# Performance work log

Hardware: AMD Instinct MI355X
Metric: run time of the kernel (lower is better)

Reference implementation:

```python
import jax, jax.numpy as jnp
import numpy as np

HEADS = 16
GROUPS = 4


def setup_inputs() -> dict:
    key = jax.random.key(0)
    k1, k2, k3, k4 = jax.random.split(key, 4)
    d_model = 2048
    d_kv = d_model * GROUPS // HEADS  # 512
    x = jax.random.normal(k1, (2, 2048, d_model), dtype=jnp.float32)
    Wq = jax.random.normal(k2, (d_model, d_model), dtype=jnp.float32) * (d_model ** -0.5)
    Wk = jax.random.normal(k3, (d_kv, d_model), dtype=jnp.float32) * (d_model ** -0.5)
    Wv = jax.random.normal(k4, (d_kv, d_model), dtype=jnp.float32) * (d_model ** -0.5)
    return {"x": x, "Wq": Wq, "Wk": Wk, "Wv": Wv}


def reference(x, Wq, Wk, Wv):
    b, t, c = x.shape
    hd = c // HEADS  # head dim
    h2g = HEADS // GROUPS  # query heads per kv group
    # projections (nn.Linear applies x @ W.T)
    q = (x @ Wq.T).reshape(b, t, HEADS, hd).transpose(0, 2, 1, 3)   # [b,H,t,hd]
    k = (x @ Wk.T).reshape(b, t, GROUPS, hd).transpose(0, 2, 1, 3)  # [b,G,t,hd]
    v = (x @ Wv.T).reshape(b, t, GROUPS, hd).transpose(0, 2, 1, 3)  # [b,G,t,hd]
    # GQA broadcast: group query heads by kv group
    qg = q.reshape(b, GROUPS, h2g, t, hd)                            # [b,G,h2g,t,hd]
    scores = jnp.einsum('bghqd,bgkd->bghqk', qg, k) * (hd ** -0.5)  # [b,G,h2g,t,t]
    causal = jnp.tril(jnp.ones((t, t), dtype=bool))
    scores = jnp.where(causal, scores, -jnp.inf)
    weights = jax.nn.softmax(scores, axis=-1)
    out = jnp.einsum('bghqk,bgkd->bghqd', weights, v)               # [b,G,h2g,t,hd]
    out = out.reshape(b, HEADS, t, hd).transpose(0, 2, 1, 3).reshape(b, t, c)
    return out
```

## Files before the change

kernel.cpp:

```cpp
#include <hip/hip_runtime.h>
#include <hip/hip_bf16.h>

typedef __bf16 bf16x8 __attribute__((ext_vector_type(8)));
typedef float f32x4 __attribute__((ext_vector_type(4)));

#define MFMA16(a,b,c) __builtin_amdgcn_mfma_f32_16x16x32_bf16(a,b,c,0,0,0)
#define GLL16(src, dst) __builtin_amdgcn_global_load_lds( \
    (const __attribute__((address_space(1))) unsigned int*)(src), \
    (__attribute__((address_space(3))) unsigned int*)(dst), 16, 0, 0)

__device__ inline unsigned int pack_bf16(float a, float b) {
    unsigned short ua = __builtin_bit_cast(unsigned short, (__bf16)a);
    unsigned short ub = __builtin_bit_cast(unsigned short, (__bf16)b);
    return ((unsigned int)ub << 16) | ua;
}
__device__ inline short bf_s(float v) {
    __bf16 b = (__bf16)v;
    return __builtin_bit_cast(short, b);
}

__global__ void cvt_all(const float* __restrict__ x,  const float* __restrict__ wq,
                        const float* __restrict__ wk, const float* __restrict__ wv,
                        __bf16* __restrict__ xb, __bf16* __restrict__ wb) {
    long i = (long)(blockIdx.x * blockDim.x + threadIdx.x) * 8;
    const float* src; __bf16* dst;
    if (i < 8388608)       { src = x  + i;              dst = xb + i; }
    else if (i < 12582912) { src = wq + (i - 8388608);  dst = wb + (i - 8388608); }
    else if (i < 13631488) { src = wk + (i - 12582912); dst = wb + (i - 12582912 + 4194304); }
    else                   { src = wv + (i - 13631488); dst = wb + (i - 13631488 + 5242880); }
    float4 a = *(const float4*)src;
    float4 b = *(const float4*)(src + 4);
    bf16x8 r;
    r[0] = (__bf16)a.x; r[1] = (__bf16)a.y; r[2] = (__bf16)a.z; r[3] = (__bf16)a.w;
    r[4] = (__bf16)b.x; r[5] = (__bf16)b.y; r[6] = (__bf16)b.z; r[7] = (__bf16)b.w;
    *(bf16x8*)dst = r;
}

__global__ __launch_bounds__(256) void gemm_qkv(const __bf16* __restrict__ A,
                                                const __bf16* __restrict__ B,
                                                __bf16* __restrict__ Qb,
                                                __bf16* __restrict__ Kf,
                                                __bf16* __restrict__ Vf,
                                                float qscale) {
    const int K = 2048;
    __shared__ __bf16 As[3 * 4096];
    __shared__ __bf16 Bs[3 * 4096];

    int tid = threadIdx.x;
    int wave = tid >> 6, lane = tid & 63;
    int quad = lane >> 4, l16 = lane & 15;

    int tm = blockIdx.x & 31, tn = blockIdx.x >> 5;

    const __bf16* Abase = A + (size_t)tm * 128 * K + (size_t)l16 * K + quad * 8;
    const __bf16* Bbase = B + (size_t)tn * 128 * K + (size_t)l16 * K + quad * 8;

    f32x4 acc[4][4] = {};

    auto stage = [&](int kt, int buf) {
#pragma unroll
        for (int rr = 0; rr < 2; ++rr) {
            int fb = rr * 4 + wave;
            GLL16(Abase + (size_t)fb * 16 * K + kt, As + buf * 4096 + fb * 512 + lane * 8);
            GLL16(Bbase + (size_t)fb * 16 * K + kt, Bs + buf * 4096 + fb * 512 + lane * 8);
        }
    };

    const int nk = K >> 5;
    stage(0, 0);
    stage(32, 1);
    asm volatile("s_waitcnt vmcnt(4)" ::: "memory");
    __builtin_amdgcn_s_barrier();

    int sl = 0, s2 = 2;
    for (int it = 0; it < nk; ++it) {
        if (it + 2 < nk) stage((it + 2) << 5, s2);
        const __bf16* Ab = As + sl * 4096;
        const __bf16* Bb = Bs + sl * 4096;
        bf16x8 af[4], bfr[4];
#pragma unroll
        for (int i = 0; i < 4; ++i)
            af[i] = *(const bf16x8*)(Ab + ((wave >> 1) * 4 + i) * 512 + lane * 8);
#pragma unroll
        for (int j = 0; j < 4; ++j)
            bfr[j] = *(const bf16x8*)(Bb + ((wave & 1) * 4 + j) * 512 + lane * 8);
#pragma unroll
        for (int i = 0; i < 4; ++i)
#pragma unroll
            for (int j = 0; j < 4; ++j)
                acc[i][j] = MFMA16(af[i], bfr[j], acc[i][j]);
        if (it + 1 < nk) {
            if (it + 2 < nk) asm volatile("s_waitcnt vmcnt(4)" ::: "memory");
            else             asm volatile("s_waitcnt vmcnt(0)" ::: "memory");
            __builtin_amdgcn_s_barrier();
        }
        sl = (sl == 2) ? 0 : sl + 1;
        s2 = (s2 == 2) ? 0 : s2 + 1;
    }

    int colbase = tn * 128 + (wave & 1) * 64;
#pragma unroll
    for (int i = 0; i < 4; ++i) {
        int row0 = tm * 128 + (wave >> 1) * 64 + i * 16 + quad * 4;
        int b = row0 >> 11, tok0 = row0 & 2047;
#pragma unroll
        for (int j = 0; j < 4; ++j) {
            int col = colbase + j * 16 + l16;
            if (tn < 16) {
#pragma unroll
                for (int r = 0; r < 4; ++r)
                    Qb[(size_t)(row0 + r) * 2048 + col] = (__bf16)(acc[i][j][r] * qscale);
            } else if (tn < 20) {
                int d_all = col - 2048;
                int g = d_all >> 7, dd = d_all & 127;
                int dt = dd >> 5, q4 = (dd >> 3) & 3, jj = dd & 7;
                int tb = tok0 >> 4, tl0 = tok0 & 15;
                __bf16* base = Kf + ((((size_t)(b * 4 + g) * 128 + tb) * 4 + dt) * 512)
                               + (q4 * 16 + tl0) * 8 + jj;
#pragma unroll
                for (int r = 0; r < 4; ++r)
                    base[r * 8] = (__bf16)acc[i][j][r];
            } else {
                int d_all = col - 2560;
                int g = d_all >> 7, dd = d_all & 127;
                int nto = dd >> 4, dl = dd & 15;
                int ch = tok0 >> 6, kk = (tok0 >> 5) & 1;
                int q4v = (tok0 >> 3) & 3, jv0 = tok0 & 7;
                size_t off = ((((size_t)(b * 4 + g) * 32 + ch) * 16) + nto * 2 + kk) * 512
                             + (q4v * 16 + dl) * 8 + jv0;
                short4 pk;
                pk.x = bf_s(acc[i][j][0]); pk.y = bf_s(acc[i][j][1]);
                pk.z = bf_s(acc[i][j][2]); pk.w = bf_s(acc[i][j][3]);
                *(short4*)(Vf + off) = pk;
            }
        }
    }
}

__global__ __launch_bounds__(256) void attn_mfma(const __bf16* __restrict__ Q,
                                                 const __bf16* __restrict__ Kf,
                                                 const __bf16* __restrict__ Vf,
                                                 float* __restrict__ O) {
    const int T = 2048, CM = 2048, HD = 128;
    __shared__ __bf16 Ks[2 * 8192];
    __shared__ __bf16 Vs[2 * 8192];
    __shared__ __bf16 Pl[8192];

    int tid = threadIdx.x;
    int wave = tid >> 6, lane = tid & 63;
    int quad = lane >> 4, l16 = lane & 15;

    int bg = blockIdx.x & 7;
    int slot = blockIdx.x >> 3;
    int qb = (slot < 32) ? (63 - slot) : (slot - 32);
    int b = bg >> 2, g = bg & 3;
    int h = g * 4 + wave;
    int q0 = qb * 32;

    bf16x8 qf[2][4];
    const __bf16* qbase = Q + (size_t)b * T * CM + (size_t)h * HD;
#pragma unroll
    for (int nt = 0; nt < 2; ++nt)
#pragma unroll
        for (int dt = 0; dt < 4; ++dt)
            qf[nt][dt] = *(const bf16x8*)(qbase + (size_t)(q0 + nt * 16 + l16) * CM
                                          + dt * 32 + quad * 8);

    const __bf16* kcb = Kf + (size_t)(b * 4 + g) * 262144;
    const __bf16* vcb = Vf + (size_t)(b * 4 + g) * 262144;

    float m_r[2] = {-1e30f, -1e30f}, l_r[2] = {0.f, 0.f};
    f32x4 o_acc[2][8] = {};
    __bf16* Pw = Pl + wave * 2048;

    auto stage_kv = [&](int ch, int buf) {
        const __bf16* kg = kcb + ch * 8192 + wave * 2048 + lane * 8;
        const __bf16* vg = vcb + ch * 8192 + wave * 2048 + lane * 8;
        __bf16* kl = Ks + buf * 8192 + wave * 2048 + lane * 8;
        __bf16* vl = Vs + buf * 8192 + wave * 2048 + lane * 8;
#pragma unroll
        for (int i = 0; i < 4; ++i) GLL16(kg + i * 512, kl + i * 512);
#pragma unroll
        for (int i = 0; i < 4; ++i) GLL16(vg + i * 512, vl + i * 512);
    };

    int nch = (qb >> 1) + 1;
    stage_kv(0, 0);
    for (int ch = 0; ch < nch; ++ch) {
        __builtin_amdgcn_s_barrier();
        if (ch + 1 < nch) {
            stage_kv(ch + 1, (ch + 1) & 1);
            asm volatile("s_waitcnt vmcnt(8)" ::: "memory");
        } else {
            asm volatile("s_waitcnt vmcnt(0)" ::: "memory");
        }
        __builtin_amdgcn_s_barrier();

        const __bf16* Kb = Ks + (ch & 1) * 8192;
        const __bf16* Vb = Vs + (ch & 1) * 8192;

        f32x4 st[2][4] = {};
#pragma unroll
        for (int t = 0; t < 4; ++t)
#pragma unroll
            for (int dt = 0; dt < 4; ++dt) {
                bf16x8 kfv = *(const bf16x8*)(Kb + (t * 4 + dt) * 512 + lane * 8);
                st[0][t] = MFMA16(kfv, qf[0][dt], st[0][t]);
                st[1][t] = MFMA16(kfv, qf[1][dt], st[1][t]);
            }

        bool diag = (ch == nch - 1);
        float alpha[2];
#pragma unroll
        for (int nt = 0; nt < 2; ++nt) {
            if (diag) {
                int qg = q0 + nt * 16 + l16;
#pragma unroll
                for (int t = 0; t < 4; ++t)
#pragma unroll
                    for (int r = 0; r < 4; ++r)
                        if (ch * 64 + t * 16 + quad * 4 + r > qg) st[nt][t][r] = -1e30f;
            }
            float cmax = -1e30f;
#pragma unroll
            for (int t = 0; t < 4; ++t)
                cmax = fmaxf(cmax, fmaxf(fmaxf(st[nt][t][0], st[nt][t][1]),
                                         fmaxf(st[nt][t][2], st[nt][t][3])));
            cmax = fmaxf(cmax, __shfl_xor(cmax, 16));
            cmax = fmaxf(cmax, __shfl_xor(cmax, 32));
            float mnew = fmaxf(m_r[nt], cmax);
            alpha[nt] = __expf(m_r[nt] - mnew);
            m_r[nt] = mnew;
            float ps = 0.f;
#pragma unroll
            for (int t = 0; t < 4; ++t) {
                float p0 = __expf(st[nt][t][0] - mnew);
                float p1 = __expf(st[nt][t][1] - mnew);
                float p2 = __expf(st[nt][t][2] - mnew);
                float p3 = __expf(st[nt][t][3] - mnew);
                ps += (p0 + p1) + (p2 + p3);
                int off = (nt * 2 + (t >> 1)) * 512 + ((t & 1) * 2 + (quad >> 1)) * 128
                          + l16 * 8 + (quad & 1) * 4;
                unsigned long long pk =
                    (unsigned long long)pack_bf16(p0, p1) |
                    ((unsigned long long)pack_bf16(p2, p3) << 32);
                *(unsigned long long*)(Pw + off) = pk;
            }
            ps += __shfl_xor(ps, 16);
            ps += __shfl_xor(ps, 32);
            l_r[nt] = l_r[nt] * alpha[nt] + ps;
        }

#pragma unroll
        for (int mt = 0; mt < 2; ++mt)
#pragma unroll
            for (int r = 0; r < 4; ++r) {
                float alr = __shfl(alpha[mt], quad * 4 + r);
#pragma unroll
                for (int nto = 0; nto < 8; ++nto)
                    o_acc[mt][nto][r] *= alr;
            }

#pragma unroll
        for (int mt = 0; mt < 2; ++mt)
#pragma unroll
            for (int kk = 0; kk < 2; ++kk) {
                bf16x8 pf = *(const bf16x8*)(Pw + (mt * 2 + kk) * 512 + lane * 8);
#pragma unroll
                for (int nto = 0; nto < 8; ++nto) {
                    bf16x8 vf = *(const bf16x8*)(Vb + (nto * 2 + kk) * 512 + lane * 8);
                    o_acc[mt][nto] = MFMA16(pf, vf, o_acc[mt][nto]);
                }
            }
    }

    float* obase = O + (size_t)b * T * CM + (size_t)h * HD;
#pragma unroll
    for (int mt = 0; mt < 2; ++mt) {
        float invl = 1.f / l_r[mt];
#pragma unroll
        for (int r = 0; r < 4; ++r) {
            float ir = __shfl(invl, quad * 4 + r);
            float* orow = obase + (size_t)(q0 + 16 * mt + quad * 4 + r) * CM;
#pragma unroll
            for (int nto = 0; nto < 8; ++nto)
                orow[nto * 16 + l16] = o_acc[mt][nto][r] * ir;
        }
    }
}

extern "C" void kernel_launch(void* const* d_in, const int* in_sizes, int n_in,
                              void* d_out, int out_size, void* d_ws, size_t ws_size,
                              hipStream_t stream) {
    const float* x  = (const float*)d_in[0];
    const float* Wq = (const float*)d_in[1];
    const float* Wk = (const float*)d_in[2];
    const float* Wv = (const float*)d_in[3];
    float* out = (float*)d_out;

    const float qscale = 0.08838834764831845f;

    __bf16* xb = (__bf16*)d_ws;
    __bf16* Wb = xb + 8388608;
    __bf16* Qb = Wb + 6291456;
    __bf16* Kfr = Qb + 8388608;
    __bf16* Vfr = Kfr + 2097152;

    cvt_all<<<7168, 256, 0, stream>>>(x, Wq, Wk, Wv, xb, Wb);
    gemm_qkv<<<768, 256, 0, stream>>>(xb, Wb, Qb, Kfr, Vfr, qscale);
    attn_mfma<<<512, 256, 0, stream>>>(Qb, Kfr, Vfr, out);
}
```

Measured before the change: 280.3 us.

## Restructure QKV GEMM into 256x256 tiles with 8 waves and phased ping-pong schedule

The QKV projection GEMM moves from 128x128 tiles with 4 waves and a 3-stage buffer to 256x256 tiles with 8 waves, BK=64 and double buffering. Each K step is split into four quadrant MFMA phases, with global-to-LDS loads interleaved between them and barriers plus s_setprio raising priority around the MFMA bursts. The aim is more operand reuse per loaded byte and overlap of loads with matrix math. The attention kernel also gets setprio around its MFMA sections and barriers fenced against compiler reordering. The grid drops to 192 blocks, which may underfill the 256 CUs, and the larger tile raises register and LDS pressure.

```diff
diff --git a/kernel.cpp b/kernel.cpp
--- a/kernel.cpp
+++ b/kernel.cpp
@@ -8,6 +8,8 @@
 #define GLL16(src, dst) __builtin_amdgcn_global_load_lds( \
     (const __attribute__((address_space(1))) unsigned int*)(src), \
     (__attribute__((address_space(3))) unsigned int*)(dst), 16, 0, 0)
+#define FENCE() asm volatile("" ::: "memory")
+#define BARRIER() do { FENCE(); __builtin_amdgcn_s_barrier(); FENCE(); } while (0)
 
 __device__ inline unsigned int pack_bf16(float a, float b) {
     unsigned short ua = __builtin_bit_cast(unsigned short, (__bf16)a);
@@ -36,101 +38,170 @@
     *(bf16x8*)dst = r;
 }
 
-__global__ __launch_bounds__(256) void gemm_qkv(const __bf16* __restrict__ A,
-                                                const __bf16* __restrict__ B,
-                                                __bf16* __restrict__ Qb,
-                                                __bf16* __restrict__ Kf,
-                                                __bf16* __restrict__ Vf,
-                                                float qscale) {
+__global__ __launch_bounds__(512, 2) void gemm_qkv(const __bf16* __restrict__ A,
+                                                   const __bf16* __restrict__ B,
+                                                   __bf16* __restrict__ Qb,
+                                                   __bf16* __restrict__ Kf,
+                                                   __bf16* __restrict__ Vf,
+                                                   float qscale) {
     const int K = 2048;
-    __shared__ __bf16 As[3 * 4096];
-    __shared__ __bf16 Bs[3 * 4096];
+    const int NT = 32;
+    __shared__ __bf16 As[2 * 16384];
+    __shared__ __bf16 Bs[2 * 16384];
 
     int tid = threadIdx.x;
     int wave = tid >> 6, lane = tid & 63;
     int quad = lane >> 4, l16 = lane & 15;
-
-    int tm = blockIdx.x & 31, tn = blockIdx.x >> 5;
-
-    const __bf16* Abase = A + (size_t)tm * 128 * K + (size_t)l16 * K + quad * 8;
-    const __bf16* Bbase = B + (size_t)tn * 128 * K + (size_t)l16 * K + quad * 8;
-
-    f32x4 acc[4][4] = {};
-
-    auto stage = [&](int kt, int buf) {
-#pragma unroll
-        for (int rr = 0; rr < 2; ++rr) {
-            int fb = rr * 4 + wave;
-            GLL16(Abase + (size_t)fb * 16 * K + kt, As + buf * 4096 + fb * 512 + lane * 8);
-            GLL16(Bbase + (size_t)fb * 16 * K + kt, Bs + buf * 4096 + fb * 512 + lane * 8);
+    int wr = wave >> 2, wc = wave & 3;
+
+    int tm = blockIdx.x & 15, tn = blockIdx.x >> 4;
+
+    const __bf16* Ab = A + (size_t)tm * 256 * K + (size_t)l16 * K + quad * 8;
+    const __bf16* Bb = B + (size_t)tn * 256 * K + (size_t)l16 * K + quad * 8;
+
+    auto stageA = [&](int kt, int buf, int mq) {
+#pragma unroll
+        for (int r = 0; r < 2; ++r) {
+            int j = r * 8 + wave;
+            int mi = j >> 1, ks = j & 1;
+            int mb = (mi & 3) + ((mi >> 2) << 3) + mq * 4;
+            GLL16(Ab + (size_t)mb * 16 * K + kt + ks * 32,
+                  As + buf * 16384 + (mb * 2 + ks) * 512 + lane * 8);
         }
     };
-
-    const int nk = K >> 5;
-    stage(0, 0);
-    stage(32, 1);
-    asm volatile("s_waitcnt vmcnt(4)" ::: "memory");
-    __builtin_amdgcn_s_barrier();
-
-    int sl = 0, s2 = 2;
-    for (int it = 0; it < nk; ++it) {
-        if (it + 2 < nk) stage((it + 2) << 5, s2);
-        const __bf16* Ab = As + sl * 4096;
-        const __bf16* Bb = Bs + sl * 4096;
-        bf16x8 af[4], bfr[4];
-#pragma unroll
-        for (int i = 0; i < 4; ++i)
-            af[i] = *(const bf16x8*)(Ab + ((wave >> 1) * 4 + i) * 512 + lane * 8);
-#pragma unroll
-        for (int j = 0; j < 4; ++j)
-            bfr[j] = *(const bf16x8*)(Bb + ((wave & 1) * 4 + j) * 512 + lane * 8);
-#pragma unroll
-        for (int i = 0; i < 4; ++i)
-#pragma unroll
-            for (int j = 0; j < 4; ++j)
-                acc[i][j] = MFMA16(af[i], bfr[j], acc[i][j]);
-        if (it + 1 < nk) {
-            if (it + 2 < nk) asm volatile("s_waitcnt vmcnt(4)" ::: "memory");
-            else             asm volatile("s_waitcnt vmcnt(0)" ::: "memory");
-            __builtin_amdgcn_s_barrier();
-        }
-        sl = (sl == 2) ? 0 : sl + 1;
-        s2 = (s2 == 2) ? 0 : s2 + 1;
+    auto stageB = [&](int kt, int buf, int nq) {
+#pragma unroll
+        for (int r = 0; r < 2; ++r) {
+            int j = r * 8 + wave;
+            int ni = j >> 1, ks = j & 1;
+            int nb = (ni & 1) + ((ni >> 1) << 2) + nq * 2;
+            GLL16(Bb + (size_t)nb * 16 * K + kt + ks * 32,
+                  Bs + buf * 16384 + (nb * 2 + ks) * 512 + lane * 8);
+        }
+    };
+
+    f32x4 acc[8][4] = {};
+
+    stageA(0, 0, 0); stageB(0, 0, 0); stageA(0, 0, 1); stageB(0, 0, 1);
+    stageA(64, 1, 0); stageB(64, 1, 0); stageA(64, 1, 1); stageB(64, 1, 1);
+    asm volatile("s_waitcnt vmcnt(8)" ::: "memory");
+    BARRIER();
+
+    for (int t = 0; t < NT; ++t) {
+        const __bf16* Ac = As + (t & 1) * 16384;
+        const __bf16* Bc = Bs + (t & 1) * 16384;
+        int kt2 = (t + 2) << 6;
+        bool st = (t + 2) < NT;
+        int bn = t & 1;
+
+        bf16x8 a0[4][2], a1[4][2], b0[2][2], b1[2][2];
+
+#pragma unroll
+        for (int m = 0; m < 4; ++m)
+#pragma unroll
+            for (int ks = 0; ks < 2; ++ks)
+                a0[m][ks] = *(const bf16x8*)(Ac + ((wr * 8 + m) * 2 + ks) * 512 + lane * 8);
+#pragma unroll
+        for (int n = 0; n < 2; ++n)
+#pragma unroll
+            for (int ks = 0; ks < 2; ++ks)
+                b0[n][ks] = *(const bf16x8*)(Bc + ((wc * 4 + n) * 2 + ks) * 512 + lane * 8);
+        BARRIER();
+        __builtin_amdgcn_s_setprio(1);
+#pragma unroll
+        for (int m = 0; m < 4; ++m)
+#pragma unroll
+            for (int n = 0; n < 2; ++n)
+#pragma unroll
+                for (int ks = 0; ks < 2; ++ks)
+                    acc[m][n] = MFMA16(a0[m][ks], b0[n][ks], acc[m][n]);
+        __builtin_amdgcn_s_setprio(0);
+        BARRIER();
+
+#pragma unroll
+        for (int m = 0; m < 4; ++m)
+#pragma unroll
+            for (int ks = 0; ks < 2; ++ks)
+                a1[m][ks] = *(const bf16x8*)(Ac + ((wr * 8 + 4 + m) * 2 + ks) * 512 + lane * 8);
+        if (st) { stageA(kt2, bn, 0); stageB(kt2, bn, 0); }
+        BARRIER();
+        __builtin_amdgcn_s_setprio(1);
+#pragma unroll
+        for (int m = 0; m < 4; ++m)
+#pragma unroll
+            for (int n = 0; n < 2; ++n)
+#pragma unroll
+                for (int ks = 0; ks < 2; ++ks)
+                    acc[4 + m][n] = MFMA16(a1[m][ks], b0[n][ks], acc[4 + m][n]);
+        __builtin_amdgcn_s_setprio(0);
+        BARRIER();
+
+#pragma unroll
+        for (int n = 0; n < 2; ++n)
+#pragma unroll
+            for (int ks = 0; ks < 2; ++ks)
+                b1[n][ks] = *(const bf16x8*)(Bc + ((wc * 4 + 2 + n) * 2 + ks) * 512 + lane * 8);
+        if (st) stageA(kt2, bn, 1);
+        BARRIER();
+        __builtin_amdgcn_s_setprio(1);
+#pragma unroll
+        for (int m = 0; m < 4; ++m)
+#pragma unroll
+            for (int n = 0; n < 2; ++n)
+#pragma unroll
+                for (int ks = 0; ks < 2; ++ks)
+                    acc[m][2 + n] = MFMA16(a0[m][ks], b1[n][ks], acc[m][2 + n]);
+        __builtin_amdgcn_s_setprio(0);
+        BARRIER();
+
+        if (st) stageB(kt2, bn, 1);
+        BARRIER();
+        __builtin_amdgcn_s_setprio(1);
+#pragma unroll
+        for (int m = 0; m < 4; ++m)
+#pragma unroll
+            for (int n = 0; n < 2; ++n)
+#pragma unroll
+                for (int ks = 0; ks < 2; ++ks)
+                    acc[4 + m][2 + n] = MFMA16(a1[m][ks], b1[n][ks], acc[4 + m][2 + n]);
+        __builtin_amdgcn_s_setprio(0);
+        if (t < NT - 2)       asm volatile("s_waitcnt vmcnt(8)" ::: "memory");
+        else if (t == NT - 2) asm volatile("s_waitcnt vmcnt(0)" ::: "memory");
+        BARRIER();
     }
 
-    int colbase = tn * 128 + (wave & 1) * 64;
-#pragma unroll
-    for (int i = 0; i < 4; ++i) {
-        int row0 = tm * 128 + (wave >> 1) * 64 + i * 16 + quad * 4;
-        int b = row0 >> 11, tok0 = row0 & 2047;
-#pragma unroll
-        for (int j = 0; j < 4; ++j) {
-            int col = colbase + j * 16 + l16;
-            if (tn < 16) {
+#pragma unroll
+    for (int m = 0; m < 8; ++m) {
+        int row0 = tm * 256 + wr * 128 + m * 16 + quad * 4;
+        int bb = row0 >> 11, tok0 = row0 & 2047;
+#pragma unroll
+        for (int n = 0; n < 4; ++n) {
+            int col = tn * 256 + wc * 64 + n * 16 + l16;
+            if (tn < 8) {
 #pragma unroll
                 for (int r = 0; r < 4; ++r)
-                    Qb[(size_t)(row0 + r) * 2048 + col] = (__bf16)(acc[i][j][r] * qscale);
-            } else if (tn < 20) {
+                    Qb[(size_t)(row0 + r) * 2048 + col] = (__bf16)(acc[m][n][r] * qscale);
+            } else if (tn < 10) {
                 int d_all = col - 2048;
                 int g = d_all >> 7, dd = d_all & 127;
                 int dt = dd >> 5, q4 = (dd >> 3) & 3, jj = dd & 7;
                 int tb = tok0 >> 4, tl0 = tok0 & 15;
-                __bf16* base = Kf + ((((size_t)(b * 4 + g) * 128 + tb) * 4 + dt) * 512)
+                __bf16* base = Kf + ((((size_t)(bb * 4 + g) * 128 + tb) * 4 + dt) * 512)
                                + (q4 * 16 + tl0) * 8 + jj;
 #pragma unroll
                 for (int r = 0; r < 4; ++r)
-                    base[r * 8] = (__bf16)acc[i][j][r];
+                    base[r * 8] = (__bf16)acc[m][n][r];
             } else {
                 int d_all = col - 2560;
                 int g = d_all >> 7, dd = d_all & 127;
                 int nto = dd >> 4, dl = dd & 15;
                 int ch = tok0 >> 6, kk = (tok0 >> 5) & 1;
                 int q4v = (tok0 >> 3) & 3, jv0 = tok0 & 7;
-                size_t off = ((((size_t)(b * 4 + g) * 32 + ch) * 16) + nto * 2 + kk) * 512
+                size_t off = ((((size_t)(bb * 4 + g) * 32 + ch) * 16) + nto * 2 + kk) * 512
                              + (q4v * 16 + dl) * 8 + jv0;
                 short4 pk;
-                pk.x = bf_s(acc[i][j][0]); pk.y = bf_s(acc[i][j][1]);
-                pk.z = bf_s(acc[i][j][2]); pk.w = bf_s(acc[i][j][3]);
+                pk.x = bf_s(acc[m][n][0]); pk.y = bf_s(acc[m][n][1]);
+                pk.z = bf_s(acc[m][n][2]); pk.w = bf_s(acc[m][n][3]);
                 *(short4*)(Vf + off) = pk;
             }
         }
@@ -187,19 +258,20 @@
     int nch = (qb >> 1) + 1;
     stage_kv(0, 0);
     for (int ch = 0; ch < nch; ++ch) {
-        __builtin_amdgcn_s_barrier();
+        BARRIER();
         if (ch + 1 < nch) {
             stage_kv(ch + 1, (ch + 1) & 1);
             asm volatile("s_waitcnt vmcnt(8)" ::: "memory");
         } else {
             asm volatile("s_waitcnt vmcnt(0)" ::: "memory");
         }
-        __builtin_amdgcn_s_barrier();
+        BARRIER();
 
         const __bf16* Kb = Ks + (ch & 1) * 8192;
         const __bf16* Vb = Vs + (ch & 1) * 8192;
 
         f32x4 st[2][4] = {};
+        __builtin_amdgcn_s_setprio(1);
 #pragma unroll
         for (int t = 0; t < 4; ++t)
 #pragma unroll
@@ -208,6 +280,7 @@
                 st[0][t] = MFMA16(kfv, qf[0][dt], st[0][t]);
                 st[1][t] = MFMA16(kfv, qf[1][dt], st[1][t]);
             }
+        __builtin_amdgcn_s_setprio(0);
 
         bool diag = (ch == nch - 1);
         float alpha[2];
@@ -261,6 +334,7 @@
                     o_acc[mt][nto][r] *= alr;
             }
 
+        __builtin_amdgcn_s_setprio(1);
 #pragma unroll
         for (int mt = 0; mt < 2; ++mt)
 #pragma unroll
@@ -272,6 +346,7 @@
                     o_acc[mt][nto] = MFMA16(pf, vf, o_acc[mt][nto]);
                 }
             }
+        __builtin_amdgcn_s_setprio(0);
     }
 
     float* obase = O + (size_t)b * T * CM + (size_t)h * HD;
@@ -307,6 +382,6 @@
     __bf16* Vfr = Kfr + 2097152;
 
     cvt_all<<<7168, 256, 0, stream>>>(x, Wq, Wk, Wv, xb, Wb);
-    gemm_qkv<<<768, 256, 0, stream>>>(xb, Wb, Qb, Kfr, Vfr, qscale);
+    gemm_qkv<<<192, 512, 0, stream>>>(xb, Wb, Qb, Kfr, Vfr, qscale);
     attn_mfma<<<512, 256, 0, stream>>>(Qb, Kfr, Vfr, out);
 }
```

Result: faster. 271.6 us (-3.1%).

## Enlarge QKV GEMM tiles to 256x256 with 8 waves; add MFMA priority hints

Applied to the files above, without the earlier changes.

The QKV projection GEMM moves from 128x128 tiles with 4 waves to 256x256 tiles with 8 waves (512 threads, 192 blocks), and each wave now computes an 8x4 grid of MFMA tiles. The goal is more operand reuse per LDS load and less global traffic per output. In exchange, the grid shrinks to 192 blocks on a 256-CU part, leaving some CUs idle, and register pressure rises. The attention kernel also wraps its MFMA sections in s_setprio to favour matrix issue across waves, and the waitcnt asm drops its memory clobber.

```diff
diff --git a/kernel.cpp b/kernel.cpp
--- a/kernel.cpp
+++ b/kernel.cpp
@@ -8,6 +8,8 @@
 #define GLL16(src, dst) __builtin_amdgcn_global_load_lds( \
     (const __attribute__((address_space(1))) unsigned int*)(src), \
     (__attribute__((address_space(3))) unsigned int*)(dst), 16, 0, 0)
+#define WAIT_VM(n)  asm volatile("s_waitcnt vmcnt(" #n ")")
+#define BAR() __builtin_amdgcn_s_barrier()
 
 __device__ inline unsigned int pack_bf16(float a, float b) {
     unsigned short ua = __builtin_bit_cast(unsigned short, (__bf16)a);
@@ -36,101 +38,101 @@
     *(bf16x8*)dst = r;
 }
 
-__global__ __launch_bounds__(256) void gemm_qkv(const __bf16* __restrict__ A,
-                                                const __bf16* __restrict__ B,
-                                                __bf16* __restrict__ Qb,
-                                                __bf16* __restrict__ Kf,
-                                                __bf16* __restrict__ Vf,
-                                                float qscale) {
+__global__ __launch_bounds__(512, 2) void gemm_qkv(const __bf16* __restrict__ A,
+                                                   const __bf16* __restrict__ B,
+                                                   __bf16* __restrict__ Qb,
+                                                   __bf16* __restrict__ Kf,
+                                                   __bf16* __restrict__ Vf,
+                                                   float qscale) {
     const int K = 2048;
-    __shared__ __bf16 As[3 * 4096];
-    __shared__ __bf16 Bs[3 * 4096];
+    const int NT = 64;
+    __shared__ __bf16 As[3 * 8192];
+    __shared__ __bf16 Bs[3 * 8192];
 
     int tid = threadIdx.x;
     int wave = tid >> 6, lane = tid & 63;
     int quad = lane >> 4, l16 = lane & 15;
-
-    int tm = blockIdx.x & 31, tn = blockIdx.x >> 5;
-
-    const __bf16* Abase = A + (size_t)tm * 128 * K + (size_t)l16 * K + quad * 8;
-    const __bf16* Bbase = B + (size_t)tn * 128 * K + (size_t)l16 * K + quad * 8;
-
-    f32x4 acc[4][4] = {};
+    int wr = wave >> 2, wc = wave & 3;
+
+    int tm = blockIdx.x & 15, tn = blockIdx.x >> 4;
+
+    const __bf16* Ab = A + (size_t)tm * 256 * K + (size_t)l16 * K + quad * 8;
+    const __bf16* Bb = B + (size_t)tn * 256 * K + (size_t)l16 * K + quad * 8;
 
     auto stage = [&](int kt, int buf) {
 #pragma unroll
-        for (int rr = 0; rr < 2; ++rr) {
-            int fb = rr * 4 + wave;
-            GLL16(Abase + (size_t)fb * 16 * K + kt, As + buf * 4096 + fb * 512 + lane * 8);
-            GLL16(Bbase + (size_t)fb * 16 * K + kt, Bs + buf * 4096 + fb * 512 + lane * 8);
+        for (int r = 0; r < 2; ++r) {
+            int mb = r * 8 + wave;
+            GLL16(Ab + (size_t)mb * 16 * K + kt, As + buf * 8192 + mb * 512 + lane * 8);
+            GLL16(Bb + (size_t)mb * 16 * K + kt, Bs + buf * 8192 + mb * 512 + lane * 8);
         }
     };
 
-    const int nk = K >> 5;
+    f32x4 acc[8][4] = {};
+
     stage(0, 0);
     stage(32, 1);
-    asm volatile("s_waitcnt vmcnt(4)" ::: "memory");
-    __builtin_amdgcn_s_barrier();
-
-    int sl = 0, s2 = 2;
-    for (int it = 0; it < nk; ++it) {
-        if (it + 2 < nk) stage((it + 2) << 5, s2);
-        const __bf16* Ab = As + sl * 4096;
-        const __bf16* Bb = Bs + sl * 4096;
-        bf16x8 af[4], bfr[4];
-#pragma unroll
-        for (int i = 0; i < 4; ++i)
-            af[i] = *(const bf16x8*)(Ab + ((wave >> 1) * 4 + i) * 512 + lane * 8);
-#pragma unroll
-        for (int j = 0; j < 4; ++j)
-            bfr[j] = *(const bf16x8*)(Bb + ((wave & 1) * 4 + j) * 512 + lane * 8);
-#pragma unroll
-        for (int i = 0; i < 4; ++i)
-#pragma unroll
-            for (int j = 0; j < 4; ++j)
-                acc[i][j] = MFMA16(af[i], bfr[j], acc[i][j]);
-        if (it + 1 < nk) {
-            if (it + 2 < nk) asm volatile("s_waitcnt vmcnt(4)" ::: "memory");
-            else             asm volatile("s_waitcnt vmcnt(0)" ::: "memory");
-            __builtin_amdgcn_s_barrier();
-        }
-        sl = (sl == 2) ? 0 : sl + 1;
-        s2 = (s2 == 2) ? 0 : s2 + 1;
+    WAIT_VM(4);
+    BAR();
+
+    int cur = 0, nxt = 2;
+    for (int t = 0; t < NT; ++t) {
+        if (t + 2 < NT) stage((t + 2) << 5, nxt);
+
+        const __bf16* Ac = As + cur * 8192;
+        const __bf16* Bc = Bs + cur * 8192;
+        bf16x8 a[8], b[4];
+#pragma unroll
+        for (int m = 0; m < 8; ++m)
+            a[m] = *(const bf16x8*)(Ac + (wr * 8 + m) * 512 + lane * 8);
+#pragma unroll
+        for (int n = 0; n < 4; ++n)
+            b[n] = *(const bf16x8*)(Bc + (wc * 4 + n) * 512 + lane * 8);
+#pragma unroll
+        for (int m = 0; m < 8; ++m)
+#pragma unroll
+            for (int n = 0; n < 4; ++n)
+                acc[m][n] = MFMA16(a[m], b[n], acc[m][n]);
+
+        if (t + 2 < NT)      WAIT_VM(4);
+        else if (t + 1 < NT) WAIT_VM(0);
+        BAR();
+        cur = (cur == 2) ? 0 : cur + 1;
+        nxt = (nxt == 2) ? 0 : nxt + 1;
     }
 
-    int colbase = tn * 128 + (wave & 1) * 64;
-#pragma unroll
-    for (int i = 0; i < 4; ++i) {
-        int row0 = tm * 128 + (wave >> 1) * 64 + i * 16 + quad * 4;
-        int b = row0 >> 11, tok0 = row0 & 2047;
-#pragma unroll
-        for (int j = 0; j < 4; ++j) {
-            int col = colbase + j * 16 + l16;
-            if (tn < 16) {
+#pragma unroll
+    for (int m = 0; m < 8; ++m) {
+        int row0 = tm * 256 + wr * 128 + m * 16 + quad * 4;
+        int bb = row0 >> 11, tok0 = row0 & 2047;
+#pragma unroll
+        for (int n = 0; n < 4; ++n) {
+            int col = tn * 256 + wc * 64 + n * 16 + l16;
+            if (tn < 8) {
 #pragma unroll
                 for (int r = 0; r < 4; ++r)
-                    Qb[(size_t)(row0 + r) * 2048 + col] = (__bf16)(acc[i][j][r] * qscale);
-            } else if (tn < 20) {
+                    Qb[(size_t)(row0 + r) * 2048 + col] = (__bf16)(acc[m][n][r] * qscale);
+            } else if (tn < 10) {
                 int d_all = col - 2048;
                 int g = d_all >> 7, dd = d_all & 127;
                 int dt = dd >> 5, q4 = (dd >> 3) & 3, jj = dd & 7;
                 int tb = tok0 >> 4, tl0 = tok0 & 15;
-                __bf16* base = Kf + ((((size_t)(b * 4 + g) * 128 + tb) * 4 + dt) * 512)
+                __bf16* base = Kf + ((((size_t)(bb * 4 + g) * 128 + tb) * 4 + dt) * 512)
                                + (q4 * 16 + tl0) * 8 + jj;
 #pragma unroll
                 for (int r = 0; r < 4; ++r)
-                    base[r * 8] = (__bf16)acc[i][j][r];
+                    base[r * 8] = (__bf16)acc[m][n][r];
             } else {
                 int d_all = col - 2560;
                 int g = d_all >> 7, dd = d_all & 127;
                 int nto = dd >> 4, dl = dd & 15;
                 int ch = tok0 >> 6, kk = (tok0 >> 5) & 1;
                 int q4v = (tok0 >> 3) & 3, jv0 = tok0 & 7;
-                size_t off = ((((size_t)(b * 4 + g) * 32 + ch) * 16) + nto * 2 + kk) * 512
+                size_t off = ((((size_t)(bb * 4 + g) * 32 + ch) * 16) + nto * 2 + kk) * 512
                              + (q4v * 16 + dl) * 8 + jv0;
                 short4 pk;
-                pk.x = bf_s(acc[i][j][0]); pk.y = bf_s(acc[i][j][1]);
-                pk.z = bf_s(acc[i][j][2]); pk.w = bf_s(acc[i][j][3]);
+                pk.x = bf_s(acc[m][n][0]); pk.y = bf_s(acc[m][n][1]);
+                pk.z = bf_s(acc[m][n][2]); pk.w = bf_s(acc[m][n][3]);
                 *(short4*)(Vf + off) = pk;
             }
         }
@@ -187,19 +189,20 @@
     int nch = (qb >> 1) + 1;
     stage_kv(0, 0);
     for (int ch = 0; ch < nch; ++ch) {
-        __builtin_amdgcn_s_barrier();
+        BAR();
         if (ch + 1 < nch) {
             stage_kv(ch + 1, (ch + 1) & 1);
-            asm volatile("s_waitcnt vmcnt(8)" ::: "memory");
+            WAIT_VM(8);
         } else {
-            asm volatile("s_waitcnt vmcnt(0)" ::: "memory");
-        }
-        __builtin_amdgcn_s_barrier();
+            WAIT_VM(0);
+        }
+        BAR();
 
         const __bf16* Kb = Ks + (ch & 1) * 8192;
         const __bf16* Vb = Vs + (ch & 1) * 8192;
 
         f32x4 st[2][4] = {};
+        __builtin_amdgcn_s_setprio(1);
 #pragma unroll
         for (int t = 0; t < 4; ++t)
 #pragma unroll
@@ -208,6 +211,7 @@
                 st[0][t] = MFMA16(kfv, qf[0][dt], st[0][t]);
                 st[1][t] = MFMA16(kfv, qf[1][dt], st[1][t]);
             }
+        __builtin_amdgcn_s_setprio(0);
 
         bool diag = (ch == nch - 1);
         float alpha[2];
@@ -261,6 +265,7 @@
                     o_acc[mt][nto][r] *= alr;
             }
 
+        __builtin_amdgcn_s_setprio(1);
 #pragma unroll
         for (int mt = 0; mt < 2; ++mt)
 #pragma unroll
@@ -272,6 +277,7 @@
                     o_acc[mt][nto] = MFMA16(pf, vf, o_acc[mt][nto]);
                 }
             }
+        __builtin_amdgcn_s_setprio(0);
     }
 
     float* obase = O + (size_t)b * T * CM + (size_t)h * HD;
@@ -307,6 +313,6 @@
     __bf16* Vfr = Kfr + 2097152;
 
     cvt_all<<<7168, 256, 0, stream>>>(x, Wq, Wk, Wv, xb, Wb);
-    gemm_qkv<<<768, 256, 0, stream>>>(xb, Wb, Qb, Kfr, Vfr, qscale);
+    gemm_qkv<<<192, 512, 0, stream>>>(xb, Wb, Qb, Kfr, Vfr, qscale);
     attn_mfma<<<512, 256, 0, stream>>>(Qb, Kfr, Vfr, out);
 }
```

Result: slower. 287.4 us (+2.5%).
